# Performance work log

Hardware: AMD Instinct MI355X
Metric: run time of the kernel (lower is better)

## Reference

```python
import jax, jax.numpy as jnp
import numpy as np
from jax import lax

B, N = 16, 4096


def _fps(xyz, npoint):
    # xyz: [N,3] -> [npoint] int32 indices (iterative farthest point sampling, start at idx 0)
    n = xyz.shape[0]
    def step(carry, _):
        dist, far = carry
        d = jnp.sum((xyz - xyz[far]) ** 2, axis=-1)
        dist = jnp.minimum(dist, d)
        nxt = jnp.argmax(dist).astype(jnp.int32)
        return (dist, nxt), far
    (_, _), idx = lax.scan(step, (jnp.full((n,), 1e10, xyz.dtype), jnp.int32(0)), None, length=npoint)
    return idx


def _ball_query(xyz, new_xyz, radius, nsample):
    # xyz: [N,3], new_xyz: [S,3] -> [S, nsample] neighbor indices within radius
    n = xyz.shape[0]
    sqr = jnp.sum((new_xyz[:, None, :] - xyz[None, :, :]) ** 2, axis=-1)  # [S,N]
    idx = jnp.where(sqr > radius * radius, n, jnp.arange(n)[None, :])
    idx = jnp.sort(idx, axis=-1)[:, :nsample]
    return jnp.where(idx == n, idx[:, :1], idx)  # pad misses with first hit


def _gather(p, i):
    return p[i]


def _mlp(feat, ws):
    # feat: [B,S,K,C]; 1x1 conv + folded eval-BN + ReLU per layer
    for W, b in ws:
        feat = jax.nn.relu(jnp.einsum('bskc,oc->bsko', feat, W) + b)
    return feat


def _sa(xyz, points, npoint, radius, nsample, ws):
    fps_idx = jax.vmap(_fps, in_axes=(0, None))(xyz, npoint)              # [B,S]
    new_xyz = jnp.take_along_axis(xyz, fps_idx[..., None], axis=1)         # [B,S,3]
    idx = jax.vmap(_ball_query, in_axes=(0, 0, None, None))(xyz, new_xyz, radius, nsample)  # [B,S,K]
    grouped_xyz = jax.vmap(_gather)(xyz, idx) - new_xyz[:, :, None, :]     # [B,S,K,3]
    if points is None:
        feat = grouped_xyz
    else:
        feat = jnp.concatenate([grouped_xyz, jax.vmap(_gather)(points, idx)], axis=-1)
    return new_xyz, jnp.max(_mlp(feat, ws), axis=2)                        # [B,S,Cout]


def _forward(x, ws1, ws2, ws3, fw, fb):
    b = x.shape[0]
    l1_xyz, l1_pts = _sa(x, None, 512, 0.2, 32, ws1)       # [B,512,3], [B,512,128]
    l2_xyz, l2_pts = _sa(l1_xyz, l1_pts, 128, 0.4, 64, ws2)  # [B,128,3], [B,128,256]
    feat = jnp.concatenate([l2_xyz, l2_pts], axis=-1)[:, None]  # group_all: [B,1,128,259]
    g = jnp.max(_mlp(feat, ws3), axis=2).reshape(b, 1024)
    return g @ fw.T + fb


_SPECS = [
    ('sa1_w0', (64, 3)), ('sa1_b0', (64,)), ('sa1_w1', (64, 64)), ('sa1_b1', (64,)), ('sa1_w2', (128, 64)), ('sa1_b2', (128,)),
    ('sa2_w0', (128, 131)), ('sa2_b0', (128,)), ('sa2_w1', (128, 128)), ('sa2_b1', (128,)), ('sa2_w2', (256, 128)), ('sa2_b2', (256,)),
    ('sa3_w0', (256, 259)), ('sa3_b0', (256,)), ('sa3_w1', (512, 256)), ('sa3_b1', (512,)), ('sa3_w2', (1024, 512)), ('sa3_b2', (1024,)),
    ('fw', (1024, 1024)), ('fb', (1024,)),
]


def setup_inputs() -> dict:
    key = jax.random.key(0)
    keys = jax.random.split(key, len(_SPECS) + 1)
    inp = {'x': jax.random.uniform(keys[0], (B, N, 3), dtype=jnp.float32)}
    for (name, shp), k in zip(_SPECS, keys[1:]):
        inp[name] = jax.random.normal(k, shp, dtype=jnp.float32) * 0.02
    return inp


def reference(x, sa1_w0, sa1_b0, sa1_w1, sa1_b1, sa1_w2, sa1_b2,
              sa2_w0, sa2_b0, sa2_w1, sa2_b1, sa2_w2, sa2_b2,
              sa3_w0, sa3_b0, sa3_w1, sa3_b1, sa3_w2, sa3_b2, fw, fb):
    ws1 = [(sa1_w0, sa1_b0), (sa1_w1, sa1_b1), (sa1_w2, sa1_b2)]
    ws2 = [(sa2_w0, sa2_b0), (sa2_w1, sa2_b1), (sa2_w2, sa2_b2)]
    ws3 = [(sa3_w0, sa3_b0), (sa3_w1, sa3_b1), (sa3_w2, sa3_b2)]
    return _forward(x, ws1, ws2, ws3, fw, fb)
```

## Files before the change

kernel.cpp:

```cpp
#include <hip/hip_runtime.h>

#ifndef BATCH
#define BATCH 16
#endif

typedef float f32x2 __attribute__((ext_vector_type(2)));
__device__ __forceinline__ f32x2 mk2(float a, float b) { f32x2 r; r.x = a; r.y = b; return r; }

template<int CTRL>
__device__ __forceinline__ float dppmaxf(float v)
{
    const int d = __builtin_amdgcn_update_dpp(__float_as_int(v), __float_as_int(v),
                                              CTRL, 0xf, 0xf, false);
    return fmaxf(v, __int_as_float(d));
}
template<int CTRL>
__device__ __forceinline__ unsigned dppminu(unsigned v)
{
    const unsigned d = (unsigned)__builtin_amdgcn_update_dpp((int)v, (int)v,
                                                             CTRL, 0xf, 0xf, false);
    return (d < v) ? d : v;
}
__device__ __forceinline__ float wave_max_bcast(float v)
{
    v = dppmaxf<0x111>(v);
    v = dppmaxf<0x112>(v);
    v = dppmaxf<0x114>(v);
    v = dppmaxf<0x118>(v);
    v = dppmaxf<0x142>(v);
    v = dppmaxf<0x143>(v);
    return __int_as_float(__builtin_amdgcn_readlane(__float_as_int(v), 63));
}
__device__ __forceinline__ unsigned wave_min_bcast(unsigned v)
{
    v = dppminu<0x111>(v);
    v = dppminu<0x112>(v);
    v = dppminu<0x114>(v);
    v = dppminu<0x118>(v);
    v = dppminu<0x142>(v);
    v = dppminu<0x143>(v);
    return (unsigned)__builtin_amdgcn_readlane((int)v, 63);
}

__device__ __forceinline__ void transpose_body(int blk, int tid,
    const float* __restrict__ s0, float* __restrict__ d0,
    const float* __restrict__ s1, float* __restrict__ d1,
    const float* __restrict__ s2, float* __restrict__ d2,
    const float* __restrict__ s3, float* __restrict__ d3,
    const float* __restrict__ s4, float* __restrict__ d4,
    const float* __restrict__ s5, float* __restrict__ d5,
    const float* __restrict__ s6, float* __restrict__ d6,
    const float* __restrict__ s7, float* __restrict__ d7,
    const float* __restrict__ s8, float* __restrict__ d8)
{
    int i = blk * 256 + tid;
    if (i < 192)    { d0[(i%3)  *64   + i/3  ] = s0[i]; return; }  i -= 192;
    if (i < 4096)   { d1[(i&63) *64   + (i>>6)] = s1[i]; return; } i -= 4096;
    if (i < 8192)   { d2[(i&63) *128  + (i>>6)] = s2[i]; return; } i -= 8192;
    if (i < 16768)  { d3[(i%131)*128  + i/131] = s3[i]; return; }  i -= 16768;
    if (i < 16384)  { d4[(i&127)*128  + (i>>7)] = s4[i]; return; } i -= 16384;
    if (i < 32768)  { d5[(i&127)*256  + (i>>7)] = s5[i]; return; } i -= 32768;
    if (i < 66304)  { d6[(i%259)*256  + i/259] = s6[i]; return; }  i -= 66304;
    if (i < 131072) { d7[(i&255)*512  + (i>>8)] = s7[i]; return; } i -= 131072;
    if (i < 524288) { d8[(i&511)*1024 + (i>>9)] = s8[i]; return; }
}

template<int N, int NP1, int NP2, int BLOCK>
__global__ __launch_bounds__(BLOCK)
void fps_fused(const float* __restrict__ xyz,
               float* __restrict__ out1, float* __restrict__ out2,
               const float* __restrict__ ts0, float* __restrict__ td0,
               const float* __restrict__ ts1, float* __restrict__ td1,
               const float* __restrict__ ts2, float* __restrict__ td2,
               const float* __restrict__ ts3, float* __restrict__ td3,
               const float* __restrict__ ts4, float* __restrict__ td4,
               const float* __restrict__ ts5, float* __restrict__ td5,
               const float* __restrict__ ts6, float* __restrict__ td6,
               const float* __restrict__ ts7, float* __restrict__ td7,
               const float* __restrict__ ts8, float* __restrict__ td8)
{
#pragma clang fp contract(off)
    if ((int)blockIdx.x >= BATCH) {
        transpose_body(blockIdx.x - BATCH, threadIdx.x,
                       ts0, td0, ts1, td1, ts2, td2, ts3, td3, ts4, td4,
                       ts5, td5, ts6, td6, ts7, td7, ts8, td8);
        return;
    }
    constexpr int P  = N / BLOCK;
    constexpr int P2 = NP1 / BLOCK;
    constexpr int NW = BLOCK / 64;
    __shared__ float sx[N], sy[N], sz[N];
    __shared__ float s2x[NP1], s2y[NP1], s2z[NP1];
    __shared__ float o2x[NP2], o2y[NP2], o2z[NP2];
    __shared__ unsigned long long wslot[2][NW];
    const int b = blockIdx.x, t = threadIdx.x;
    const int lane = t & 63, wv = t >> 6;
    const float* xb = xyz + (size_t)b * N * 3;
    float px[P], py[P], pz[P], dist[P];
#pragma unroll
    for (int j = 0; j < P; ++j) {
        const int i = t + j * BLOCK;
        const float x = xb[i*3+0], y = xb[i*3+1], z = xb[i*3+2];
        sx[i] = x; sy[i] = y; sz[i] = z;
        px[j] = x; py[j] = y; pz[j] = z;
        dist[j] = 1e10f;
    }
    __syncthreads();
    float fx = sx[0], fy = sy[0], fz = sz[0];
    if (t == 0) { s2x[0] = fx; s2y[0] = fy; s2z[0] = fz; }
    for (int s = 1; s < NP1; ++s) {
        float bestv = -1.f; int besti = 0;
#pragma unroll
        for (int j = 0; j < P; ++j) {
            const float dx = px[j]-fx, dy = py[j]-fy, dz = pz[j]-fz;
            const float d = (dx*dx + dy*dy) + dz*dz;
            const float nd = fminf(dist[j], d);
            dist[j] = nd;
            if (nd > bestv) { bestv = nd; besti = t + j * BLOCK; }
        }
        const float wm = wave_max_bcast(bestv);
        const unsigned cand = (bestv == wm) ? (unsigned)besti : 0xffffffffu;
        const unsigned wi = wave_min_bcast(cand);
        const int par = s & 1;
        if (lane == 0)
            wslot[par][wv] = ((unsigned long long)__float_as_uint(wm) << 32)
                           | (unsigned)(~wi);
        __syncthreads();
        unsigned long long pa = wslot[par][0];
#pragma unroll
        for (int w = 1; w < NW; ++w) {
            const unsigned long long pb = wslot[par][w];
            pa = (pb > pa) ? pb : pa;
        }
        const int far = (int)(~(unsigned)pa);
        fx = sx[far]; fy = sy[far]; fz = sz[far];
        if (t == 0) { s2x[s] = fx; s2y[s] = fy; s2z[s] = fz; }
    }
    __syncthreads();
    float mx[P2], my[P2], mz[P2], d2[P2];
#pragma unroll
    for (int j = 0; j < P2; ++j) {
        const int i = t + j * BLOCK;
        mx[j] = s2x[i]; my[j] = s2y[i]; mz[j] = s2z[i];
        d2[j] = 1e10f;
    }
    fx = s2x[0]; fy = s2y[0]; fz = s2z[0];
    if (t == 0) { o2x[0] = fx; o2y[0] = fy; o2z[0] = fz; }
    for (int s = 1; s < NP2; ++s) {
        float bestv = -1.f; int besti = 0;
#pragma unroll
        for (int j = 0; j < P2; ++j) {
            const float dx = mx[j]-fx, dy = my[j]-fy, dz = mz[j]-fz;
            const float d = (dx*dx + dy*dy) + dz*dz;
            const float nd = fminf(d2[j], d);
            d2[j] = nd;
            if (nd > bestv) { bestv = nd; besti = t + j * BLOCK; }
        }
        const float wm = wave_max_bcast(bestv);
        const unsigned cand = (bestv == wm) ? (unsigned)besti : 0xffffffffu;
        const unsigned wi = wave_min_bcast(cand);
        const int par = s & 1;
        if (lane == 0)
            wslot[par][wv] = ((unsigned long long)__float_as_uint(wm) << 32)
                           | (unsigned)(~wi);
        __syncthreads();
        unsigned long long pa = wslot[par][0];
#pragma unroll
        for (int w = 1; w < NW; ++w) {
            const unsigned long long pb = wslot[par][w];
            pa = (pb > pa) ? pb : pa;
        }
        const int far2 = (int)(~(unsigned)pa);
        fx = s2x[far2]; fy = s2y[far2]; fz = s2z[far2];
        if (t == 0) { o2x[s] = fx; o2y[s] = fy; o2z[s] = fz; }
    }
    __syncthreads();
    for (int i = t; i < NP1; i += BLOCK) {
        out1[((size_t)b*NP1 + i)*3 + 0] = s2x[i];
        out1[((size_t)b*NP1 + i)*3 + 1] = s2y[i];
        out1[((size_t)b*NP1 + i)*3 + 2] = s2z[i];
    }
    for (int i = t; i < NP2; i += BLOCK) {
        out2[((size_t)b*NP2 + i)*3 + 0] = o2x[i];
        out2[((size_t)b*NP2 + i)*3 + 1] = o2y[i];
        out2[((size_t)b*NP2 + i)*3 + 2] = o2z[i];
    }
}

template<int N, int K>
__device__ __forceinline__ void ballq_scan_lds(const float* __restrict__ xb,
                                               const float qx, const float qy,
                                               const float qz, const float r2,
                                               int* __restrict__ sidx,
                                               const int lane)
{
#pragma clang fp contract(off)
    int base = 0, first = -1;
    for (int c = 0; c < N; c += 64) {
        const int i = c + lane;
        const float dx = xb[i*3+0]-qx, dy = xb[i*3+1]-qy, dz = xb[i*3+2]-qz;
        const float d = (dx*dx + dy*dy) + dz*dz;
        const bool hit = !(d > r2);
        const unsigned long long m = __ballot(hit);
        if (first < 0 && m) first = c + __builtin_ctzll(m);
        const int pos = base + __popcll(m & ((1ull << lane) - 1ull));
        if (hit && pos < K) sidx[pos] = i;
        base += __popcll(m);
        if (base >= K) break;
    }
    if (base < K && lane >= base && lane < K) sidx[lane] = first;
}

__device__ __forceinline__ void fma16pk(f32x2 (&acc)[8], const float f,
                                        const float* __restrict__ wrow)
{
    const float4 w0 = ((const float4*)wrow)[0];
    const float4 w1 = ((const float4*)wrow)[1];
    const float4 w2 = ((const float4*)wrow)[2];
    const float4 w3 = ((const float4*)wrow)[3];
    const f32x2 ff = mk2(f, f);
    acc[0] += ff * mk2(w0.x, w0.y);
    acc[1] += ff * mk2(w0.z, w0.w);
    acc[2] += ff * mk2(w1.x, w1.y);
    acc[3] += ff * mk2(w1.z, w1.w);
    acc[4] += ff * mk2(w2.x, w2.y);
    acc[5] += ff * mk2(w2.z, w2.w);
    acc[6] += ff * mk2(w3.x, w3.y);
    acc[7] += ff * mk2(w3.z, w3.w);
}

__device__ __forceinline__ float pool_half(float v)
{
    v = fmaxf(v, __shfl_xor(v, 1));
    v = fmaxf(v, __shfl_xor(v, 2));
    v = fmaxf(v, __shfl_xor(v, 4));
    v = fmaxf(v, __shfl_xor(v, 8));
    v = fmaxf(v, __shfl_xor(v, 16));
    return v;
}
__device__ __forceinline__ float pool_full(float v)
{
    v = pool_half(v);
    return fmaxf(v, __shfl_xor(v, 32));
}

__global__ __launch_bounds__(256)
void sa1_fused(const float* __restrict__ xyz, const float* __restrict__ nxyz,
               const float r2,
               const float* __restrict__ Wt0, const float* __restrict__ B0,
               const float* __restrict__ Wt1, const float* __restrict__ B1,
               const float* __restrict__ Wt2, const float* __restrict__ B2,
               float* __restrict__ out)
{
    __shared__ float buf[64][64];
    __shared__ int sidx[64];
    const int tid = threadIdx.x, lane = tid & 63;
    const int wave = __builtin_amdgcn_readfirstlane(tid >> 6);
    const int row0 = blockIdx.x * 64;
    const int g0 = row0 >> 5;
    const int b = g0 >> 9;
    const float* xb = xyz + (size_t)b * 4096 * 3;
    if (wave < 2) {
        const int g = g0 + wave;
        ballq_scan_lds<4096, 32>(xb,
            nxyz[(size_t)g*3 + 0], nxyz[(size_t)g*3 + 1], nxyz[(size_t)g*3 + 2],
            r2, sidx + wave*32, lane);
    }
    __syncthreads();
    const int g = g0 + (lane >> 5);
    const int i = sidx[lane];
    const float* p = xb + (size_t)i * 3;
    const float f0 = p[0] - nxyz[(size_t)g*3 + 0];
    const float f1 = p[1] - nxyz[(size_t)g*3 + 1];
    const float f2 = p[2] - nxyz[(size_t)g*3 + 2];
    const int oc0 = wave * 16;
    f32x2 aL[8], aH[8];
#pragma unroll
    for (int j = 0; j < 16; ++j) {
        const float v = B0[oc0+j] + f0*Wt0[0*64+oc0+j] + f1*Wt0[1*64+oc0+j] + f2*Wt0[2*64+oc0+j];
        buf[oc0+j][lane] = fmaxf(v, 0.f);
    }
    __syncthreads();
#pragma unroll
    for (int k = 0; k < 8; ++k) aL[k] = mk2(B1[oc0+2*k], B1[oc0+2*k+1]);
#pragma unroll 4
    for (int ci = 0; ci < 64; ++ci)
        fma16pk(aL, buf[ci][lane], Wt1 + ci*64 + oc0);
    __syncthreads();
#pragma unroll
    for (int k = 0; k < 8; ++k) {
        buf[oc0+2*k][lane]   = fmaxf(aL[k].x, 0.f);
        buf[oc0+2*k+1][lane] = fmaxf(aL[k].y, 0.f);
    }
    __syncthreads();
#pragma unroll
    for (int k = 0; k < 8; ++k) {
        aL[k] = mk2(B2[oc0+2*k], B2[oc0+2*k+1]);
        aH[k] = mk2(B2[64+oc0+2*k], B2[64+oc0+2*k+1]);
    }
#pragma unroll 2
    for (int ci = 0; ci < 64; ++ci) {
        const float f = buf[ci][lane];
        fma16pk(aL, f, Wt2 + ci*128 + oc0);
        fma16pk(aH, f, Wt2 + ci*128 + 64 + oc0);
    }
#pragma unroll
    for (int k = 0; k < 8; ++k) {
        const float v0 = pool_half(fmaxf(aL[k].x, 0.f));
        const float v1 = pool_half(fmaxf(aL[k].y, 0.f));
        const float w0 = pool_half(fmaxf(aH[k].x, 0.f));
        const float w1 = pool_half(fmaxf(aH[k].y, 0.f));
        if ((lane & 31) == 0) {
            const size_t orow = (size_t)((row0 + lane) >> 5) * 128;
            out[orow + oc0 + 2*k]       = v0;
            out[orow + oc0 + 2*k + 1]   = v1;
            out[orow + 64 + oc0 + 2*k]     = w0;
            out[orow + 64 + oc0 + 2*k + 1] = w1;
        }
    }
}

__global__ __launch_bounds__(256)
void sa2_fused(const float* __restrict__ l1xyz, const float* __restrict__ l1pts,
               const float* __restrict__ nxyz, const float r2,
               const float* __restrict__ Wt0, const float* __restrict__ B0,
               const float* __restrict__ Wt1, const float* __restrict__ B1,
               const float* __restrict__ Wt2, const float* __restrict__ B2,
               const float* __restrict__ Wt30, const float* __restrict__ B30,
               const float* __restrict__ Wt31, const float* __restrict__ B31,
               float* __restrict__ outH2)
{
    __shared__ float buf[128][64];
    __shared__ float pool[256];
    __shared__ float h1s[256];
    __shared__ int sidx[64];
    const int tid = threadIdx.x, lane = tid & 63;
    const int wave = __builtin_amdgcn_readfirstlane(tid >> 6);
    const int gblk = blockIdx.x;
    const int b = gblk >> 7;
    const float cx = nxyz[(size_t)gblk*3 + 0];
    const float cy = nxyz[(size_t)gblk*3 + 1];
    const float cz = nxyz[(size_t)gblk*3 + 2];
    const float* xb = l1xyz + (size_t)b * 512 * 3;
    if (wave == 0)
        ballq_scan_lds<512, 64>(xb, cx, cy, cz, r2, sidx, lane);
    __syncthreads();
    const int myi = sidx[lane];
    const float* pc = xb + (size_t)myi * 3;
    const float f0 = pc[0] - cx;
    const float f1 = pc[1] - cy;
    const float f2 = pc[2] - cz;
    for (int r = wave; r < 64; r += 4) {
        const int i2 = sidx[r];
        const float* src = l1pts + ((size_t)b*512 + i2) * 128;
        buf[lane][r ^ lane]    = src[lane];
        buf[lane+64][r ^ lane] = src[lane + 64];
    }
    __syncthreads();
    const int oc0 = wave * 16;
    f32x2 aL[8], aH[8];
#pragma unroll
    for (int k = 0; k < 8; ++k) {
        const int j0 = oc0 + 2*k, j1 = oc0 + 2*k + 1;
        aL[k] = mk2(B0[j0]    + f0*Wt0[j0]     + f1*Wt0[128+j0]    + f2*Wt0[256+j0],
                    B0[j1]    + f0*Wt0[j1]     + f1*Wt0[128+j1]    + f2*Wt0[256+j1]);
        aH[k] = mk2(B0[64+j0] + f0*Wt0[64+j0]  + f1*Wt0[192+j0]    + f2*Wt0[320+j0],
                    B0[64+j1] + f0*Wt0[64+j1]  + f1*Wt0[192+j1]    + f2*Wt0[320+j1]);
    }
#pragma unroll 2
    for (int ci = 0; ci < 128; ++ci) {
        const float f = buf[ci][lane ^ (ci & 63)];
        const float* wp = Wt0 + (size_t)(ci+3)*128;
        fma16pk(aL, f, wp + oc0);
        fma16pk(aH, f, wp + 64 + oc0);
    }
    __syncthreads();
#pragma unroll
    for (int k = 0; k < 8; ++k) {
        buf[oc0+2*k][lane]      = fmaxf(aL[k].x, 0.f);
        buf[oc0+2*k+1][lane]    = fmaxf(aL[k].y, 0.f);
        buf[64+oc0+2*k][lane]   = fmaxf(aH[k].x, 0.f);
        buf[64+oc0+2*k+1][lane] = fmaxf(aH[k].y, 0.f);
    }
    __syncthreads();
#pragma unroll
    for (int k = 0; k < 8; ++k) {
        aL[k] = mk2(B1[oc0+2*k], B1[oc0+2*k+1]);
        aH[k] = mk2(B1[64+oc0+2*k], B1[64+oc0+2*k+1]);
    }
#pragma unroll 2
    for (int ci = 0; ci < 128; ++ci) {
        const float f = buf[ci][lane];
        const float* wp = Wt1 + (size_t)ci*128;
        fma16pk(aL, f, wp + oc0);
        fma16pk(aH, f, wp + 64 + oc0);
    }
    __syncthreads();
#pragma unroll
    for (int k = 0; k < 8; ++k) {
        buf[oc0+2*k][lane]      = fmaxf(aL[k].x, 0.f);
        buf[oc0+2*k+1][lane]    = fmaxf(aL[k].y, 0.f);
        buf[64+oc0+2*k][lane]   = fmaxf(aH[k].x, 0.f);
        buf[64+oc0+2*k+1][lane] = fmaxf(aH[k].y, 0.f);
    }
    __syncthreads();
    for (int half = 0; half < 2; ++half) {
        const int oc = half*128 + oc0;
#pragma unroll
        for (int k = 0; k < 8; ++k) {
            aL[k] = mk2(B2[oc+2*k], B2[oc+2*k+1]);
            aH[k] = mk2(B2[64+oc+2*k], B2[64+oc+2*k+1]);
        }
#pragma unroll 2
        for (int ci = 0; ci < 128; ++ci) {
            const float f = buf[ci][lane];
            const float* wp = Wt2 + (size_t)ci*256;
            fma16pk(aL, f, wp + oc);
            fma16pk(aH, f, wp + 64 + oc);
        }
#pragma unroll
        for (int k = 0; k < 8; ++k) {
            const float v0 = pool_full(fmaxf(aL[k].x, 0.f));
            const float v1 = pool_full(fmaxf(aL[k].y, 0.f));
            const float w0 = pool_full(fmaxf(aH[k].x, 0.f));
            const float w1 = pool_full(fmaxf(aH[k].y, 0.f));
            if (lane == 0) {
                pool[oc + 2*k]        = v0;
                pool[oc + 2*k + 1]    = v1;
                pool[64 + oc + 2*k]   = w0;
                pool[64 + oc + 2*k+1] = w1;
            }
        }
    }
    __syncthreads();
    {
        float acc = B30[tid] + cx*Wt30[0*256+tid] + cy*Wt30[1*256+tid] + cz*Wt30[2*256+tid];
#pragma unroll 8
        for (int ci = 0; ci < 256; ++ci)
            acc += pool[ci] * Wt30[(size_t)(ci+3)*256 + tid];
        h1s[tid] = fmaxf(acc, 0.f);
    }
    __syncthreads();
    {
        float a0 = B31[tid], a1 = B31[256 + tid];
#pragma unroll 8
        for (int ci = 0; ci < 256; ++ci) {
            const float f = h1s[ci];
            a0 += f * Wt31[(size_t)ci*512 + tid];
            a1 += f * Wt31[(size_t)ci*512 + 256 + tid];
        }
        outH2[(size_t)gblk*512 + tid]       = fmaxf(a0, 0.f);
        outH2[(size_t)gblk*512 + 256 + tid] = fmaxf(a1, 0.f);
    }
}

template<int CIN, int COUT, bool CONCAT3, bool POOL>
__global__ __launch_bounds__(256)
void mlp_gemm_kernel(const float* __restrict__ inA, const float* __restrict__ inB,
                     const float* __restrict__ Wt, const float* __restrict__ Bb,
                     float* __restrict__ out)
{
    __shared__ float featS[128][64];
    const int tid = threadIdx.x, lane = tid & 63;
    const int wave = __builtin_amdgcn_readfirstlane(tid >> 6);
    const int row0 = blockIdx.x * 64;
    const int oc0 = blockIdx.y * 64 + wave * 16;
    f32x2 acc[8];
#pragma unroll
    for (int k = 0; k < 8; ++k) acc[k] = mk2(Bb[oc0+2*k], Bb[oc0+2*k+1]);
    for (int c0 = 0; c0 < CIN; c0 += 128) {
        const int csz = (CIN - c0 < 128) ? (CIN - c0) : 128;
        __syncthreads();
        for (int r = wave; r < 64; r += 4) {
            const int row = row0 + r;
            for (int cl = lane; cl < csz; cl += 64) {
                const int cig = c0 + cl;
                float v;
                if (CONCAT3)
                    v = (cig < 3) ? inA[(size_t)row*3 + cig]
                                  : inB[(size_t)row*(CIN-3) + (cig - 3)];
                else
                    v = inA[(size_t)row*CIN + cig];
                featS[cl][r ^ (cl & 63)] = v;
            }
        }
        __syncthreads();
        if (csz == 128) {
#pragma unroll 4
            for (int ci = 0; ci < 128; ++ci)
                fma16pk(acc, featS[ci][lane ^ (ci & 63)], Wt + (size_t)(c0+ci)*COUT + oc0);
        } else {
            for (int ci = 0; ci < csz; ++ci)
                fma16pk(acc, featS[ci][lane ^ (ci & 63)], Wt + (size_t)(c0+ci)*COUT + oc0);
        }
    }
    if (POOL) {
#pragma unroll
        for (int k = 0; k < 8; ++k) {
            const float v0 = pool_full(fmaxf(acc[k].x, 0.f));
            const float v1 = pool_full(fmaxf(acc[k].y, 0.f));
            if (lane == 0) {
                out[(size_t)blockIdx.x * COUT + oc0 + 2*k]     = v0;
                out[(size_t)blockIdx.x * COUT + oc0 + 2*k + 1] = v1;
            }
        }
    } else {
        float4 o0, o1, o2, o3;
        o0.x=fmaxf(acc[0].x,0.f); o0.y=fmaxf(acc[0].y,0.f); o0.z=fmaxf(acc[1].x,0.f); o0.w=fmaxf(acc[1].y,0.f);
        o1.x=fmaxf(acc[2].x,0.f); o1.y=fmaxf(acc[2].y,0.f); o1.z=fmaxf(acc[3].x,0.f); o1.w=fmaxf(acc[3].y,0.f);
        o2.x=fmaxf(acc[4].x,0.f); o2.y=fmaxf(acc[4].y,0.f); o2.z=fmaxf(acc[5].x,0.f); o2.w=fmaxf(acc[5].y,0.f);
        o3.x=fmaxf(acc[6].x,0.f); o3.y=fmaxf(acc[6].y,0.f); o3.z=fmaxf(acc[7].x,0.f); o3.w=fmaxf(acc[7].y,0.f);
        float4* op = (float4*)(out + (size_t)(row0 + lane)*COUT + oc0);
        op[0]=o0; op[1]=o1; op[2]=o2; op[3]=o3;
    }
}

__global__ __launch_bounds__(256)
void fc_kernel(const float* __restrict__ pmax, const float* __restrict__ fw,
               const float* __restrict__ fb, float* __restrict__ y)
{
    const int gw = (blockIdx.x * 256 + threadIdx.x) >> 6;
    const int lane = threadIdx.x & 63;
    const int b = gw >> 10, o = gw & 1023;
    const float4* g0 = (const float4*)(pmax + (size_t)(2*b) * 1024);
    const float4* g1 = (const float4*)(pmax + (size_t)(2*b+1) * 1024);
    const float4* wv = (const float4*)(fw + (size_t)o * 1024);
    float acc = 0.f;
#pragma unroll
    for (int r = 0; r < 4; ++r) {
        const float4 a = g0[lane + r*64];
        const float4 c = g1[lane + r*64];
        const float4 w = wv[lane + r*64];
        acc += fmaxf(a.x,c.x)*w.x + fmaxf(a.y,c.y)*w.y
             + fmaxf(a.z,c.z)*w.z + fmaxf(a.w,c.w)*w.w;
    }
#pragma unroll
    for (int m = 32; m >= 1; m >>= 1) acc += __shfl_xor(acc, m);
    if (lane == 0) y[gw] = acc + fb[o];
}

extern "C" void kernel_launch(void* const* d_in, const int* in_sizes, int n_in,
                              void* d_out, int out_size, void* d_ws, size_t ws_size,
                              hipStream_t stream)
{
    (void)in_sizes; (void)n_in; (void)out_size; (void)ws_size;
    const float* x   = (const float*)d_in[0];
    const float* s1w0 = (const float*)d_in[1];  const float* s1b0 = (const float*)d_in[2];
    const float* s1w1 = (const float*)d_in[3];  const float* s1b1 = (const float*)d_in[4];
    const float* s1w2 = (const float*)d_in[5];  const float* s1b2 = (const float*)d_in[6];
    const float* s2w0 = (const float*)d_in[7];  const float* s2b0 = (const float*)d_in[8];
    const float* s2w1 = (const float*)d_in[9];  const float* s2b1 = (const float*)d_in[10];
    const float* s2w2 = (const float*)d_in[11]; const float* s2b2 = (const float*)d_in[12];
    const float* s3w0 = (const float*)d_in[13]; const float* s3b0 = (const float*)d_in[14];
    const float* s3w1 = (const float*)d_in[15]; const float* s3b1 = (const float*)d_in[16];
    const float* s3w2 = (const float*)d_in[17]; const float* s3b2 = (const float*)d_in[18];
    const float* fw  = (const float*)d_in[19]; const float* fb  = (const float*)d_in[20];
    float* y = (float*)d_out;

    char* ws = (char*)d_ws;
    float* l1_xyz = (float*)(ws + 0);
    float* l1_pts = (float*)(ws + 1146880);
    float* l2_xyz = (float*)(ws + 5341184);
    float* h2     = (float*)(ws + 10084352);
    float* pmax   = (float*)(ws + 14278656);
    float* wt1_0  = (float*)(ws + 14409728);
    float* wt1_1  = (float*)(ws + 14410496);
    float* wt1_2  = (float*)(ws + 14426880);
    float* wt2_0  = (float*)(ws + 14459648);
    float* wt2_1  = (float*)(ws + 14526720);
    float* wt2_2  = (float*)(ws + 14592256);
    float* wt3_0  = (float*)(ws + 14723328);
    float* wt3_1  = (float*)(ws + 14988544);
    float* wt3_2  = (float*)(ws + 15512832);

    const float r2_1 = (float)(0.2 * 0.2);
    const float r2_2 = (float)(0.4 * 0.4);

    fps_fused<4096, 512, 128, 256><<<BATCH + 3126, 256, 0, stream>>>(
        x, l1_xyz, l2_xyz,
        s1w0, wt1_0, s1w1, wt1_1, s1w2, wt1_2,
        s2w0, wt2_0, s2w1, wt2_1, s2w2, wt2_2,
        s3w0, wt3_0, s3w1, wt3_1, s3w2, wt3_2);
    sa1_fused<<<(BATCH*512*32)/64, 256, 0, stream>>>(x, l1_xyz, r2_1,
        wt1_0, s1b0, wt1_1, s1b1, wt1_2, s1b2, l1_pts);
    sa2_fused<<<BATCH*128, 256, 0, stream>>>(l1_xyz, l1_pts, l2_xyz, r2_2,
        wt2_0, s2b0, wt2_1, s2b1, wt2_2, s2b2,
        wt3_0, s3b0, wt3_1, s3b1, h2);
    mlp_gemm_kernel<512, 1024, false, true ><<<dim3(32, 16), 256, 0, stream>>>(h2, nullptr, wt3_2, s3b2, pmax);
    fc_kernel<<<(BATCH*1024)/4, 256, 0, stream>>>(pmax, fw, fb, y);
}
```

Before: 862.8 us.

## Move second-level FPS into SA1 kernel to overlap with grouping MLP

The second farthest-point-sampling pass (128 of 512 points) moves out of the first FPS kernel into extra blocks of the SA1 grouping/MLP kernel. Those 16 serial FPS blocks can then run alongside the thousands of SA1 blocks instead of lengthening the serial FPS1 critical path. Shared memory is now a raw byte buffer reinterpreted per role. The risk is that the long-running FPS2 blocks finish last and become a tail, and that the larger shared allocation lowers SA1 occupancy.

```diff
diff --git a/kernel.cpp b/kernel.cpp
--- a/kernel.cpp
+++ b/kernel.cpp
@@ -65,19 +65,18 @@
     if (i < 524288) { d8[(i&511)*1024 + (i>>9)] = s8[i]; return; }
 }
 
-template<int N, int NP1, int NP2, int BLOCK>
+template<int N, int NP1, int BLOCK>
 __global__ __launch_bounds__(BLOCK)
-void fps_fused(const float* __restrict__ xyz,
-               float* __restrict__ out1, float* __restrict__ out2,
-               const float* __restrict__ ts0, float* __restrict__ td0,
-               const float* __restrict__ ts1, float* __restrict__ td1,
-               const float* __restrict__ ts2, float* __restrict__ td2,
-               const float* __restrict__ ts3, float* __restrict__ td3,
-               const float* __restrict__ ts4, float* __restrict__ td4,
-               const float* __restrict__ ts5, float* __restrict__ td5,
-               const float* __restrict__ ts6, float* __restrict__ td6,
-               const float* __restrict__ ts7, float* __restrict__ td7,
-               const float* __restrict__ ts8, float* __restrict__ td8)
+void fps1_fused(const float* __restrict__ xyz, float* __restrict__ out1,
+                const float* __restrict__ ts0, float* __restrict__ td0,
+                const float* __restrict__ ts1, float* __restrict__ td1,
+                const float* __restrict__ ts2, float* __restrict__ td2,
+                const float* __restrict__ ts3, float* __restrict__ td3,
+                const float* __restrict__ ts4, float* __restrict__ td4,
+                const float* __restrict__ ts5, float* __restrict__ td5,
+                const float* __restrict__ ts6, float* __restrict__ td6,
+                const float* __restrict__ ts7, float* __restrict__ td7,
+                const float* __restrict__ ts8, float* __restrict__ td8)
 {
 #pragma clang fp contract(off)
     if ((int)blockIdx.x >= BATCH) {
@@ -87,11 +86,9 @@
         return;
     }
     constexpr int P  = N / BLOCK;
-    constexpr int P2 = NP1 / BLOCK;
     constexpr int NW = BLOCK / 64;
     __shared__ float sx[N], sy[N], sz[N];
     __shared__ float s2x[NP1], s2y[NP1], s2z[NP1];
-    __shared__ float o2x[NP2], o2y[NP2], o2z[NP2];
     __shared__ unsigned long long wslot[2][NW];
     const int b = blockIdx.x, t = threadIdx.x;
     const int lane = t & 63, wv = t >> 6;
@@ -137,53 +134,10 @@
         if (t == 0) { s2x[s] = fx; s2y[s] = fy; s2z[s] = fz; }
     }
     __syncthreads();
-    float mx[P2], my[P2], mz[P2], d2[P2];
-#pragma unroll
-    for (int j = 0; j < P2; ++j) {
-        const int i = t + j * BLOCK;
-        mx[j] = s2x[i]; my[j] = s2y[i]; mz[j] = s2z[i];
-        d2[j] = 1e10f;
-    }
-    fx = s2x[0]; fy = s2y[0]; fz = s2z[0];
-    if (t == 0) { o2x[0] = fx; o2y[0] = fy; o2z[0] = fz; }
-    for (int s = 1; s < NP2; ++s) {
-        float bestv = -1.f; int besti = 0;
-#pragma unroll
-        for (int j = 0; j < P2; ++j) {
-            const float dx = mx[j]-fx, dy = my[j]-fy, dz = mz[j]-fz;
-            const float d = (dx*dx + dy*dy) + dz*dz;
-            const float nd = fminf(d2[j], d);
-            d2[j] = nd;
-            if (nd > bestv) { bestv = nd; besti = t + j * BLOCK; }
-        }
-        const float wm = wave_max_bcast(bestv);
-        const unsigned cand = (bestv == wm) ? (unsigned)besti : 0xffffffffu;
-        const unsigned wi = wave_min_bcast(cand);
-        const int par = s & 1;
-        if (lane == 0)
-            wslot[par][wv] = ((unsigned long long)__float_as_uint(wm) << 32)
-                           | (unsigned)(~wi);
-        __syncthreads();
-        unsigned long long pa = wslot[par][0];
-#pragma unroll
-        for (int w = 1; w < NW; ++w) {
-            const unsigned long long pb = wslot[par][w];
-            pa = (pb > pa) ? pb : pa;
-        }
-        const int far2 = (int)(~(unsigned)pa);
-        fx = s2x[far2]; fy = s2y[far2]; fz = s2z[far2];
-        if (t == 0) { o2x[s] = fx; o2y[s] = fy; o2z[s] = fz; }
-    }
-    __syncthreads();
     for (int i = t; i < NP1; i += BLOCK) {
         out1[((size_t)b*NP1 + i)*3 + 0] = s2x[i];
         out1[((size_t)b*NP1 + i)*3 + 1] = s2y[i];
         out1[((size_t)b*NP1 + i)*3 + 2] = s2z[i];
-    }
-    for (int i = t; i < NP2; i += BLOCK) {
-        out2[((size_t)b*NP2 + i)*3 + 0] = o2x[i];
-        out2[((size_t)b*NP2 + i)*3 + 1] = o2y[i];
-        out2[((size_t)b*NP2 + i)*3 + 2] = o2z[i];
     }
 }
 
@@ -244,35 +198,98 @@
     return fmaxf(v, __shfl_xor(v, 32));
 }
 
-__global__ __launch_bounds__(256)
-void sa1_fused(const float* __restrict__ xyz, const float* __restrict__ nxyz,
-               const float r2,
-               const float* __restrict__ Wt0, const float* __restrict__ B0,
-               const float* __restrict__ Wt1, const float* __restrict__ B1,
-               const float* __restrict__ Wt2, const float* __restrict__ B2,
-               float* __restrict__ out)
-{
-    __shared__ float buf[64][64];
-    __shared__ int sidx[64];
+template<int NP1, int NP2, int BLOCK>
+__global__ __launch_bounds__(BLOCK)
+void fps2_sa1(const float* __restrict__ xyz, const float* __restrict__ l1xyz,
+              float* __restrict__ out2, const float r2,
+              const float* __restrict__ Wt0, const float* __restrict__ B0,
+              const float* __restrict__ Wt1, const float* __restrict__ B1,
+              const float* __restrict__ Wt2, const float* __restrict__ B2,
+              float* __restrict__ out)
+{
+#pragma clang fp contract(off)
+    __shared__ __align__(16) char smem[16640];
     const int tid = threadIdx.x, lane = tid & 63;
+    if ((int)blockIdx.x < BATCH) {
+        constexpr int P2 = NP1 / BLOCK;
+        constexpr int NW = BLOCK / 64;
+        float* s2x = (float*)smem;
+        float* s2y = s2x + NP1;
+        float* s2z = s2y + NP1;
+        float* o2x = s2z + NP1;
+        float* o2y = o2x + NP2;
+        float* o2z = o2y + NP2;
+        unsigned long long* wslot = (unsigned long long*)(o2z + NP2);
+        const int b = blockIdx.x, t = tid, wv = t >> 6;
+        const float* l1b = l1xyz + (size_t)b * NP1 * 3;
+        float mx[P2], my[P2], mz[P2], d2[P2];
+#pragma unroll
+        for (int j = 0; j < P2; ++j) {
+            const int i = t + j * BLOCK;
+            const float x = l1b[i*3+0], y = l1b[i*3+1], z = l1b[i*3+2];
+            s2x[i] = x; s2y[i] = y; s2z[i] = z;
+            mx[j] = x; my[j] = y; mz[j] = z;
+            d2[j] = 1e10f;
+        }
+        __syncthreads();
+        float fx = s2x[0], fy = s2y[0], fz = s2z[0];
+        if (t == 0) { o2x[0] = fx; o2y[0] = fy; o2z[0] = fz; }
+        for (int s = 1; s < NP2; ++s) {
+            float bestv = -1.f; int besti = 0;
+#pragma unroll
+            for (int j = 0; j < P2; ++j) {
+                const float dx = mx[j]-fx, dy = my[j]-fy, dz = mz[j]-fz;
+                const float d = (dx*dx + dy*dy) + dz*dz;
+                const float nd = fminf(d2[j], d);
+                d2[j] = nd;
+                if (nd > bestv) { bestv = nd; besti = t + j * BLOCK; }
+            }
+            const float wm = wave_max_bcast(bestv);
+            const unsigned cand = (bestv == wm) ? (unsigned)besti : 0xffffffffu;
+            const unsigned wi = wave_min_bcast(cand);
+            const int par = s & 1;
+            if (lane == 0)
+                wslot[par*NW + wv] = ((unsigned long long)__float_as_uint(wm) << 32)
+                                   | (unsigned)(~wi);
+            __syncthreads();
+            unsigned long long pa = wslot[par*NW + 0];
+#pragma unroll
+            for (int w = 1; w < NW; ++w) {
+                const unsigned long long pb = wslot[par*NW + w];
+                pa = (pb > pa) ? pb : pa;
+            }
+            const int far2 = (int)(~(unsigned)pa);
+            fx = s2x[far2]; fy = s2y[far2]; fz = s2z[far2];
+            if (t == 0) { o2x[s] = fx; o2y[s] = fy; o2z[s] = fz; }
+        }
+        __syncthreads();
+        for (int i = t; i < NP2; i += BLOCK) {
+            out2[((size_t)b*NP2 + i)*3 + 0] = o2x[i];
+            out2[((size_t)b*NP2 + i)*3 + 1] = o2y[i];
+            out2[((size_t)b*NP2 + i)*3 + 2] = o2z[i];
+        }
+        return;
+    }
+    float (*buf)[64] = (float(*)[64])smem;
+    int* sidx = (int*)(smem + 16384);
     const int wave = __builtin_amdgcn_readfirstlane(tid >> 6);
-    const int row0 = blockIdx.x * 64;
+    const int row0 = (blockIdx.x - BATCH) * 64;
     const int g0 = row0 >> 5;
     const int b = g0 >> 9;
     const float* xb = xyz + (size_t)b * 4096 * 3;
     if (wave < 2) {
         const int g = g0 + wave;
         ballq_scan_lds<4096, 32>(xb,
-            nxyz[(size_t)g*3 + 0], nxyz[(size_t)g*3 + 1], nxyz[(size_t)g*3 + 2],
+            l1xyz[(size_t)g*3 + 0], l1xyz[(size_t)g*3 + 1], l1xyz[(size_t)g*3 + 2],
             r2, sidx + wave*32, lane);
     }
     __syncthreads();
     const int g = g0 + (lane >> 5);
     const int i = sidx[lane];
     const float* p = xb + (size_t)i * 3;
-    const float f0 = p[0] - nxyz[(size_t)g*3 + 0];
-    const float f1 = p[1] - nxyz[(size_t)g*3 + 1];
-    const float f2 = p[2] - nxyz[(size_t)g*3 + 2];
+    const float f0 = p[0] - l1xyz[(size_t)g*3 + 0];
+    const float f1 = p[1] - l1xyz[(size_t)g*3 + 1];
+    const float f2 = p[2] - l1xyz[(size_t)g*3 + 2];
     const int oc0 = wave * 16;
     f32x2 aL[8], aH[8];
 #pragma unroll
@@ -576,12 +593,13 @@
     const float r2_1 = (float)(0.2 * 0.2);
     const float r2_2 = (float)(0.4 * 0.4);
 
-    fps_fused<4096, 512, 128, 256><<<BATCH + 3126, 256, 0, stream>>>(
-        x, l1_xyz, l2_xyz,
+    fps1_fused<4096, 512, 256><<<BATCH + 3126, 256, 0, stream>>>(
+        x, l1_xyz,
         s1w0, wt1_0, s1w1, wt1_1, s1w2, wt1_2,
         s2w0, wt2_0, s2w1, wt2_1, s2w2, wt2_2,
         s3w0, wt3_0, s3w1, wt3_1, s3w2, wt3_2);
-    sa1_fused<<<(BATCH*512*32)/64, 256, 0, stream>>>(x, l1_xyz, r2_1,
+    fps2_sa1<512, 128, 256><<<BATCH + (BATCH*512*32)/64, 256, 0, stream>>>(
+        x, l1_xyz, l2_xyz, r2_1,
         wt1_0, s1b0, wt1_1, s1b1, wt1_2, s1b2, l1_pts);
     sa2_fused<<<BATCH*128, 256, 0, stream>>>(l1_xyz, l1_pts, l2_xyz, r2_2,
         wt2_0, s2b0, wt2_1, s2b1, wt2_2, s2b2,
```

Measured after the change: 820.1 us. 4.9% less time.
